# Performance work log

Measured on AMD Instinct MI355X. Metric: run time of the kernel, lower is better.

Reference implementation:

```python
import jax, jax.numpy as jnp
import numpy as np

D_MODEL = 1024
NUM_HEAD = 16
D_HEAD = 64


def setup_inputs() -> dict:
    key = jax.random.key(0)
    ks = jax.random.split(key, 9)
    b, p = 8, 1024
    s = 1.0 / np.sqrt(D_MODEL)
    inp = {
        "x": jax.random.normal(ks[0], (b, p, D_MODEL), jnp.float32),
        "w_q": jax.random.uniform(ks[1], (D_MODEL, D_MODEL), jnp.float32, -s, s),
        "b_q": jax.random.uniform(ks[2], (D_MODEL,), jnp.float32, -s, s),
        "w_k": jax.random.uniform(ks[3], (D_MODEL, D_MODEL), jnp.float32, -s, s),
        "b_k": jax.random.uniform(ks[4], (D_MODEL,), jnp.float32, -s, s),
        "w_v": jax.random.uniform(ks[5], (D_MODEL, D_MODEL), jnp.float32, -s, s),
        "b_v": jax.random.uniform(ks[6], (D_MODEL,), jnp.float32, -s, s),
        "w_o": jax.random.uniform(ks[7], (D_MODEL, D_MODEL), jnp.float32, -s, s),
        "b_o": jax.random.uniform(ks[8], (D_MODEL,), jnp.float32, -s, s),
    }
    return inp


def reference(x, w_q, b_q, w_k, b_k, w_v, b_v, w_o, b_o):
    b, p, _ = x.shape
    # projections (torch Linear: y = x @ W.T + b; here weights stored [in,out])
    q = x @ w_q + b_q
    k = x @ w_k + b_k
    v = x @ w_v + b_v
    # [b, h, p, d]
    q = q.reshape(b, p, NUM_HEAD, D_HEAD).transpose(0, 2, 1, 3)
    k = k.reshape(b, p, NUM_HEAD, D_HEAD).transpose(0, 2, 1, 3)
    v = v.reshape(b, p, NUM_HEAD, D_HEAD).transpose(0, 2, 1, 3)
    scale = 1.0 / np.sqrt(D_HEAD).astype(np.float32)
    scores = jnp.einsum("bhqd,bhkd->bhqk", q, k) * scale
    attn = jax.nn.softmax(scores, axis=-1)
    out = jnp.einsum("bhqk,bhkd->bhqd", attn, v)
    out = out.transpose(0, 2, 1, 3).reshape(b, p, D_MODEL)
    return out @ w_o + b_o
```

## Files before the change

### kernel.cpp

```cpp
#include <hip/hip_runtime.h>
#include <stdint.h>


typedef __attribute__((ext_vector_type(8))) short short8;
typedef __attribute__((ext_vector_type(4))) short s16x4;
typedef __attribute__((ext_vector_type(4))) float f32x4;

__device__ __forceinline__ short f2bf(float f) {
  unsigned u = __builtin_bit_cast(unsigned, f);
  u += 0x7fffu + ((u >> 16) & 1u);
  return (short)(u >> 16);
}

__device__ __forceinline__ unsigned pk2bf(float a, float b) {
  unsigned ua = __builtin_bit_cast(unsigned, a);
  unsigned ub = __builtin_bit_cast(unsigned, b);
  ua += 0x7fffu + ((ua >> 16) & 1u);
  ub += 0x7fffu + ((ub >> 16) & 1u);
  return (ua >> 16) | (ub & 0xffff0000u);
}

__device__ __forceinline__ unsigned cvtpk(float a, float b) {
  unsigned r;
  asm("v_cvt_pk_bf16_f32 %0, %1, %2" : "=v"(r) : "v"(a), "v"(b));
  return r;
}

__device__ __forceinline__ float fexp2(float x) {
  float r;
  asm("v_exp_f32 %0, %1" : "=v"(r) : "v"(x));
  return r;
}

typedef __attribute__((address_space(3))) void lds_void;
typedef __attribute__((address_space(1))) void gbl_void;
#define GLD16(gp, lp) \
  __builtin_amdgcn_global_load_lds((gbl_void*)(gp), (lds_void*)(lp), 16, 0, 0)

#define MFMA(a, b, c) __builtin_amdgcn_mfma_f32_16x16x32_bf16((a), (b), (c), 0, 0, 0)

__global__ __launch_bounds__(256) void k_prep(const float* __restrict__ x,
                                              short* __restrict__ xb,
                                              const float* __restrict__ s0,
                                              const float* __restrict__ s1,
                                              const float* __restrict__ s2,
                                              const float* __restrict__ s3,
                                              short* __restrict__ d0,
                                              short* __restrict__ d1,
                                              short* __restrict__ d2,
                                              short* __restrict__ d3) {
  if (blockIdx.z == 4) {
    int t = threadIdx.y * 32 + threadIdx.x;
    int bid = blockIdx.y * 32 + blockIdx.x;
#pragma unroll
    for (int j = 0; j < 8; ++j) {
      int i = (bid * 2048 + j * 256 + t) * 8;
      const float4* s = (const float4*)(x + i);
      float4 f0 = s[0], f1 = s[1];
      short8 o;
      o[0] = f2bf(f0.x); o[1] = f2bf(f0.y); o[2] = f2bf(f0.z); o[3] = f2bf(f0.w);
      o[4] = f2bf(f1.x); o[5] = f2bf(f1.y); o[6] = f2bf(f1.z); o[7] = f2bf(f1.w);
      *(short8*)(xb + i) = o;
    }
    return;
  }
  __shared__ float tile[64][33];
  const float* srcs[4] = {s0, s1, s2, s3};
  short* dsts[4] = {d0, d1, d2, d3};
  const float* src = srcs[blockIdx.z];
  short* dst = dsts[blockIdx.z];
  int tx = threadIdx.x, ty = threadIdx.y;
  int x0 = blockIdx.x * 32, y0 = blockIdx.y * 64;
#pragma unroll
  for (int i = 0; i < 64; i += 8)
    tile[ty + i][tx] = src[(y0 + ty + i) * 1024 + x0 + tx];
  __syncthreads();
#pragma unroll
  for (int i = 0; i < 32; i += 8) {
    int r = ty + i;
    *(int*)&dst[(x0 + r) * 1024 + y0 + 2 * tx] =
        (int)pk2bf(tile[2 * tx][r], tile[2 * tx + 1][r]);
  }
}

template <int MODE>
__global__ __launch_bounds__(256, 3) void k_gemm(const short* __restrict__ A,
                                                 const short* __restrict__ Bt,
                                                 const float* __restrict__ bias0,
                                                 const float* __restrict__ bias1,
                                                 const float* __restrict__ bias2,
                                                 short* __restrict__ o0,
                                                 short* __restrict__ o1,
                                                 short* __restrict__ o2,
                                                 float* __restrict__ of) {
  __shared__ __align__(16) short a_lds[128 * 64];
  __shared__ __align__(16) short b_lds[128 * 64];
  const int tid = threadIdx.x;
  const int l = blockIdx.x;
  const int m0 = ((((l & 7) << 3) | ((l >> 3) & 7))) << 7;
  const int n0 = (l >> 6) << 7;
  const int w = tid >> 6;
  const int lane = tid & 63;
  const int ll = lane & 15;
  const int qd = lane >> 4;
  const int wm = (w & 1) * 64;
  const int wn = (w >> 1) * 64;

  const int srow = tid >> 3;
  const int schunk = ((tid & 7) ^ (srow & 7)) * 8;
  const short* ag = A + (long)(m0 + srow) * 1024 + schunk;
  const short* bg = Bt + (long)(n0 + srow) * 1024 + schunk;

  f32x4 acc[4][4] = {};

  for (int kt = 0; kt < 1024; kt += 64) {
#pragma unroll
    for (int j = 0; j < 4; ++j) {
      GLD16(ag + j * 32768 + kt, &a_lds[j * 2048 + tid * 8]);
      GLD16(bg + j * 32768 + kt, &b_lds[j * 2048 + tid * 8]);
    }
    __syncthreads();
#pragma unroll
    for (int kh = 0; kh < 2; ++kh) {
      const int xoff = (((kh * 4 + qd) ^ (ll & 7)) * 8);
      short8 af[4], bfr[4];
#pragma unroll
      for (int mt = 0; mt < 4; ++mt)
        af[mt] = *(const short8*)&a_lds[(wm + mt * 16 + ll) * 64 + xoff];
#pragma unroll
      for (int nt = 0; nt < 4; ++nt)
        bfr[nt] = *(const short8*)&b_lds[(wn + nt * 16 + ll) * 64 + xoff];
#pragma unroll
      for (int mt = 0; mt < 4; ++mt)
#pragma unroll
        for (int nt = 0; nt < 4; ++nt)
          acc[mt][nt] = MFMA(af[mt], bfr[nt], acc[mt][nt]);
    }
    __syncthreads();
  }

  if (MODE == 0) {
#pragma unroll
    for (int nt = 0; nt < 4; ++nt) {
      int n = n0 + wn + nt * 16 + ll;
      int which = n >> 10;
      int nl = n & 1023;
      int h = nl >> 6, d = n & 63;
      if (which == 2) {
        float bv = bias2[nl];
        const int b = m0 >> 10;
        const int p0 = (m0 & 1023) + wm;
#pragma unroll
        for (int mt = 0; mt < 4; ++mt) {
          int p = p0 + mt * 16 + qd * 4;
          int2 pk;
          pk.x = (int)pk2bf(acc[mt][nt][0] + bv, acc[mt][nt][1] + bv);
          pk.y = (int)pk2bf(acc[mt][nt][2] + bv, acc[mt][nt][3] + bv);
          *(int2*)&o2[(long)(b * 16 + h) * 65536 + d * 1024 + p] = pk;
        }
      } else {
        float bv = (which == 0) ? bias0[nl] : bias1[nl];
        float sc = (which == 0) ? 0.18033688f : 1.0f;
        short* o = (which == 0) ? o0 : o1;
#pragma unroll
        for (int mt = 0; mt < 4; ++mt) {
#pragma unroll
          for (int r = 0; r < 4; ++r) {
            int m = m0 + wm + mt * 16 + qd * 4 + r;
            int b = m >> 10, p = m & 1023;
            o[(long)(b * 16 + h) * 65536 + p * 64 + d] = f2bf((acc[mt][nt][r] + bv) * sc);
          }
        }
      }
    }
  } else {
#pragma unroll
    for (int nt = 0; nt < 4; ++nt) {
      int n = n0 + wn + nt * 16 + ll;
      float bv = bias0[n];
#pragma unroll
      for (int mt = 0; mt < 4; ++mt) {
#pragma unroll
        for (int r = 0; r < 4; ++r) {
          int m = m0 + wm + mt * 16 + qd * 4 + r;
          of[(long)m * 1024 + n] = acc[mt][nt][r] + bv;
        }
      }
    }
  }
}

__global__ __launch_bounds__(256, 4) void k_attn(const short* __restrict__ Q,
                                                 const short* __restrict__ K,
                                                 const short* __restrict__ VT,
                                                 short* __restrict__ O) {
  __shared__ __align__(16) short k_lds[2][4096];
  __shared__ __align__(16) short vt_lds[2][4096];
  const int tid = threadIdx.x;
  const int w = tid >> 6, lane = tid & 63, ll = lane & 15, qd = lane >> 4;
  const int bid = blockIdx.x;
  const int xcd = bid & 7;
  const int inner = bid >> 3;
  const int bh = xcd * 16 + (inner & 15);
  const int qb = inner >> 4;
  const long hoff = (long)bh * 65536;
  const int qr0 = qb * 128 + w * 32;

  const short* qg = Q + hoff + (long)(qr0 + ll) * 64 + qd * 8;
  short8 qf[2][2];
  qf[0][0] = *(const short8*)qg;
  qf[0][1] = *(const short8*)(qg + 32);
  qf[1][0] = *(const short8*)(qg + 1024);
  qf[1][1] = *(const short8*)(qg + 1024 + 32);

  const int sr = tid >> 3;
  const int swz = (tid & 7) ^ (sr & 7);
  const int pr = (sr & 0x23) | ((sr & 0x0C) << 1) | ((sr & 0x10) >> 2);
  const short* kg = K + hoff + pr * 64 + swz * 8;
  const short* vg = VT + hoff + (long)sr * 1024 + swz * 8;

  const int swzr = ll & 7;
  const int fro0 = ll * 64 + ((qd ^ swzr) * 8);
  const int fro1 = ll * 64 + (((4 + qd) ^ swzr) * 8);

  f32x4 oacc[2][4] = {};
  float l_part[2] = {0.f, 0.f};

  GLD16(kg, &k_lds[0][tid * 8]);
  GLD16(kg + 2048, &k_lds[0][2048 + tid * 8]);
  GLD16(vg, &vt_lds[0][tid * 8]);
  GLD16(vg + 32768, &vt_lds[0][2048 + tid * 8]);
  __syncthreads();

#pragma unroll 2
  for (int c = 0; c < 16; ++c) {
    const int cur = c & 1, nxt = cur ^ 1;
    if (c < 15) {
      GLD16(kg + (c + 1) * 4096, &k_lds[nxt][tid * 8]);
      GLD16(kg + (c + 1) * 4096 + 2048, &k_lds[nxt][2048 + tid * 8]);
      GLD16(vg + (c + 1) * 64, &vt_lds[nxt][tid * 8]);
      GLD16(vg + (c + 1) * 64 + 32768, &vt_lds[nxt][2048 + tid * 8]);
    }

    f32x4 s[2][4];
    __builtin_amdgcn_s_setprio(1);
#pragma unroll
    for (int jt = 0; jt < 4; ++jt) {
      short8 kf0 = *(const short8*)&k_lds[cur][jt * 1024 + fro0];
      short8 kf1 = *(const short8*)&k_lds[cur][jt * 1024 + fro1];
      f32x4 t0 = {};
      t0 = MFMA(kf0, qf[0][0], t0);
      t0 = MFMA(kf1, qf[0][1], t0);
      s[0][jt] = t0;
      f32x4 t1 = {};
      t1 = MFMA(kf0, qf[1][0], t1);
      t1 = MFMA(kf1, qf[1][1], t1);
      s[1][jt] = t1;
    }
    __builtin_amdgcn_s_setprio(0);

    short8 pf[2][2];
#pragma unroll
    for (int g = 0; g < 2; ++g) {
      float rs = 0.f;
#pragma unroll
      for (int jt = 0; jt < 4; ++jt)
#pragma unroll
        for (int r = 0; r < 4; ++r) {
          float e = fexp2(s[g][jt][r]);
          s[g][jt][r] = e;
          rs += e;
        }
      l_part[g] += rs;
#pragma unroll
      for (int u = 0; u < 2; ++u) {
        union { short8 v; unsigned x[4]; } pk;
        pk.x[0] = cvtpk(s[g][2 * u][0], s[g][2 * u][1]);
        pk.x[1] = cvtpk(s[g][2 * u][2], s[g][2 * u][3]);
        pk.x[2] = cvtpk(s[g][2 * u + 1][0], s[g][2 * u + 1][1]);
        pk.x[3] = cvtpk(s[g][2 * u + 1][2], s[g][2 * u + 1][3]);
        pf[g][u] = pk.v;
      }
    }

    __builtin_amdgcn_s_setprio(1);
#pragma unroll
    for (int dt = 0; dt < 4; ++dt) {
      short8 vf0 = *(const short8*)&vt_lds[cur][dt * 1024 + fro0];
      short8 vf1 = *(const short8*)&vt_lds[cur][dt * 1024 + fro1];
      oacc[0][dt] = MFMA(vf0, pf[0][0], oacc[0][dt]);
      oacc[0][dt] = MFMA(vf1, pf[0][1], oacc[0][dt]);
      oacc[1][dt] = MFMA(vf0, pf[1][0], oacc[1][dt]);
      oacc[1][dt] = MFMA(vf1, pf[1][1], oacc[1][dt]);
    }
    __builtin_amdgcn_s_setprio(0);
    __syncthreads();
  }

  const int b = bh >> 4, h = bh & 15;
#pragma unroll
  for (int g = 0; g < 2; ++g) {
    float l = l_part[g];
    l += __shfl_xor(l, 16, 64);
    l += __shfl_xor(l, 32, 64);
    const float inv = 1.0f / l;
    const long row = (long)(b * 1024 + qr0 + g * 16 + ll);
#pragma unroll
    for (int dt = 0; dt < 4; ++dt) {
      int2 ov;
      ov.x = (int)cvtpk(oacc[g][dt][0] * inv, oacc[g][dt][1] * inv);
      ov.y = (int)cvtpk(oacc[g][dt][2] * inv, oacc[g][dt][3] * inv);
      *(int2*)&O[row * 1024 + h * 64 + dt * 16 + qd * 4] = ov;
    }
  }
}

extern "C" void kernel_launch(void* const* d_in, const int* in_sizes, int n_in,
                              void* d_out, int out_size, void* d_ws, size_t ws_size,
                              hipStream_t stream) {
  const float* x   = (const float*)d_in[0];
  const float* w_q = (const float*)d_in[1];
  const float* b_q = (const float*)d_in[2];
  const float* w_k = (const float*)d_in[3];
  const float* b_k = (const float*)d_in[4];
  const float* w_v = (const float*)d_in[5];
  const float* b_v = (const float*)d_in[6];
  const float* w_o = (const float*)d_in[7];
  const float* b_o = (const float*)d_in[8];

  char* ws = (char*)d_ws;
  short* xb    = (short*)(ws);
  short* wqkvT = (short*)(ws + (16ull << 20));
  short* woT   = (short*)(ws + (22ull << 20));
  short* qw    = (short*)(ws + (24ull << 20));
  short* kw    = (short*)(ws + (40ull << 20));
  short* vw    = (short*)(ws + (56ull << 20));

  k_prep<<<dim3(32, 16, 5), dim3(32, 8), 0, stream>>>(
      x, xb, w_q, w_k, w_v, w_o,
      wqkvT, wqkvT + (1 << 20), wqkvT + (2 << 20), woT);

  k_gemm<0><<<1536, 256, 0, stream>>>(xb, wqkvT, b_q, b_k, b_v,
                                      qw, kw, vw, nullptr);

  k_attn<<<dim3(1024), 256, 0, stream>>>(qw, kw, vw, xb);

  k_gemm<1><<<512, 256, 0, stream>>>(xb, woT, b_o, nullptr, nullptr,
                                     nullptr, nullptr, nullptr, (float*)d_out);
}
```

Before: 226.3 us.

## Triple-buffer K/V tiles in attention kernel with prefetch depth two

```diff
diff --git a/kernel.cpp b/kernel.cpp
--- a/kernel.cpp
+++ b/kernel.cpp
@@ -190,12 +190,12 @@
   }
 }
 
-__global__ __launch_bounds__(256, 4) void k_attn(const short* __restrict__ Q,
+__global__ __launch_bounds__(256, 3) void k_attn(const short* __restrict__ Q,
                                                  const short* __restrict__ K,
                                                  const short* __restrict__ VT,
                                                  short* __restrict__ O) {
-  __shared__ __align__(16) short k_lds[2][4096];
-  __shared__ __align__(16) short vt_lds[2][4096];
+  __shared__ __align__(16) short k_lds[3][4096];
+  __shared__ __align__(16) short vt_lds[3][4096];
   const int tid = threadIdx.x;
   const int w = tid >> 6, lane = tid & 63, ll = lane & 15, qd = lane >> 4;
   const int bid = blockIdx.x;
@@ -226,76 +226,84 @@
   f32x4 oacc[2][4] = {};
   float l_part[2] = {0.f, 0.f};
 
-  GLD16(kg, &k_lds[0][tid * 8]);
-  GLD16(kg + 2048, &k_lds[0][2048 + tid * 8]);
-  GLD16(vg, &vt_lds[0][tid * 8]);
-  GLD16(vg + 32768, &vt_lds[0][2048 + tid * 8]);
-  __syncthreads();
-
-#pragma unroll 2
-  for (int c = 0; c < 16; ++c) {
-    const int cur = c & 1, nxt = cur ^ 1;
-    if (c < 15) {
-      GLD16(kg + (c + 1) * 4096, &k_lds[nxt][tid * 8]);
-      GLD16(kg + (c + 1) * 4096 + 2048, &k_lds[nxt][2048 + tid * 8]);
-      GLD16(vg + (c + 1) * 64, &vt_lds[nxt][tid * 8]);
-      GLD16(vg + (c + 1) * 64 + 32768, &vt_lds[nxt][2048 + tid * 8]);
-    }
-
-    f32x4 s[2][4];
-    __builtin_amdgcn_s_setprio(1);
-#pragma unroll
-    for (int jt = 0; jt < 4; ++jt) {
-      short8 kf0 = *(const short8*)&k_lds[cur][jt * 1024 + fro0];
-      short8 kf1 = *(const short8*)&k_lds[cur][jt * 1024 + fro1];
-      f32x4 t0 = {};
-      t0 = MFMA(kf0, qf[0][0], t0);
-      t0 = MFMA(kf1, qf[0][1], t0);
-      s[0][jt] = t0;
-      f32x4 t1 = {};
-      t1 = MFMA(kf0, qf[1][0], t1);
-      t1 = MFMA(kf1, qf[1][1], t1);
-      s[1][jt] = t1;
-    }
-    __builtin_amdgcn_s_setprio(0);
-
-    short8 pf[2][2];
-#pragma unroll
-    for (int g = 0; g < 2; ++g) {
-      float rs = 0.f;
-#pragma unroll
-      for (int jt = 0; jt < 4; ++jt)
-#pragma unroll
-        for (int r = 0; r < 4; ++r) {
-          float e = fexp2(s[g][jt][r]);
-          s[g][jt][r] = e;
-          rs += e;
-        }
-      l_part[g] += rs;
-#pragma unroll
-      for (int u = 0; u < 2; ++u) {
-        union { short8 v; unsigned x[4]; } pk;
-        pk.x[0] = cvtpk(s[g][2 * u][0], s[g][2 * u][1]);
-        pk.x[1] = cvtpk(s[g][2 * u][2], s[g][2 * u][3]);
-        pk.x[2] = cvtpk(s[g][2 * u + 1][0], s[g][2 * u + 1][1]);
-        pk.x[3] = cvtpk(s[g][2 * u + 1][2], s[g][2 * u + 1][3]);
-        pf[g][u] = pk.v;
-      }
-    }
-
-    __builtin_amdgcn_s_setprio(1);
-#pragma unroll
-    for (int dt = 0; dt < 4; ++dt) {
-      short8 vf0 = *(const short8*)&vt_lds[cur][dt * 1024 + fro0];
-      short8 vf1 = *(const short8*)&vt_lds[cur][dt * 1024 + fro1];
-      oacc[0][dt] = MFMA(vf0, pf[0][0], oacc[0][dt]);
-      oacc[0][dt] = MFMA(vf1, pf[0][1], oacc[0][dt]);
-      oacc[1][dt] = MFMA(vf0, pf[1][0], oacc[1][dt]);
-      oacc[1][dt] = MFMA(vf1, pf[1][1], oacc[1][dt]);
-    }
-    __builtin_amdgcn_s_setprio(0);
-    __syncthreads();
-  }
+#define ASTAGE(t, bidx)                                              \
+  {                                                                  \
+    GLD16(kg + (t) * 4096, &k_lds[bidx][tid * 8]);                   \
+    GLD16(kg + (t) * 4096 + 2048, &k_lds[bidx][2048 + tid * 8]);     \
+    GLD16(vg + (t) * 64, &vt_lds[bidx][tid * 8]);                    \
+    GLD16(vg + (t) * 64 + 32768, &vt_lds[bidx][2048 + tid * 8]);     \
+  }
+
+#define ACOMPUTE(cur)                                                        \
+  {                                                                          \
+    f32x4 s[2][4];                                                           \
+    __builtin_amdgcn_s_setprio(1);                                           \
+    _Pragma("unroll")                                                        \
+    for (int jt = 0; jt < 4; ++jt) {                                         \
+      short8 kf0 = *(const short8*)&k_lds[cur][jt * 1024 + fro0];            \
+      short8 kf1 = *(const short8*)&k_lds[cur][jt * 1024 + fro1];            \
+      f32x4 t0 = {};                                                         \
+      t0 = MFMA(kf0, qf[0][0], t0);                                          \
+      t0 = MFMA(kf1, qf[0][1], t0);                                          \
+      s[0][jt] = t0;                                                         \
+      f32x4 t1 = {};                                                         \
+      t1 = MFMA(kf0, qf[1][0], t1);                                          \
+      t1 = MFMA(kf1, qf[1][1], t1);                                          \
+      s[1][jt] = t1;                                                         \
+    }                                                                        \
+    __builtin_amdgcn_s_setprio(0);                                           \
+    short8 pf[2][2];                                                         \
+    _Pragma("unroll")                                                        \
+    for (int g = 0; g < 2; ++g) {                                            \
+      float rs = 0.f;                                                        \
+      _Pragma("unroll")                                                      \
+      for (int jt = 0; jt < 4; ++jt)                                         \
+        _Pragma("unroll")                                                    \
+        for (int r = 0; r < 4; ++r) {                                        \
+          float e = fexp2(s[g][jt][r]);                                      \
+          s[g][jt][r] = e;                                                   \
+          rs += e;                                                           \
+        }                                                                    \
+      l_part[g] += rs;                                                       \
+      _Pragma("unroll")                                                      \
+      for (int u = 0; u < 2; ++u) {                                          \
+        union { short8 v; unsigned x[4]; } pk;                               \
+        pk.x[0] = cvtpk(s[g][2 * u][0], s[g][2 * u][1]);                     \
+        pk.x[1] = cvtpk(s[g][2 * u][2], s[g][2 * u][3]);                     \
+        pk.x[2] = cvtpk(s[g][2 * u + 1][0], s[g][2 * u + 1][1]);             \
+        pk.x[3] = cvtpk(s[g][2 * u + 1][2], s[g][2 * u + 1][3]);             \
+        pf[g][u] = pk.v;                                                     \
+      }                                                                      \
+    }                                                                        \
+    __builtin_amdgcn_s_setprio(1);                                           \
+    _Pragma("unroll")                                                        \
+    for (int dt = 0; dt < 4; ++dt) {                                         \
+      short8 vf0 = *(const short8*)&vt_lds[cur][dt * 1024 + fro0];           \
+      short8 vf1 = *(const short8*)&vt_lds[cur][dt * 1024 + fro1];           \
+      oacc[0][dt] = MFMA(vf0, pf[0][0], oacc[0][dt]);                        \
+      oacc[0][dt] = MFMA(vf1, pf[0][1], oacc[0][dt]);                        \
+      oacc[1][dt] = MFMA(vf0, pf[1][0], oacc[1][dt]);                        \
+      oacc[1][dt] = MFMA(vf1, pf[1][1], oacc[1][dt]);                        \
+    }                                                                        \
+    __builtin_amdgcn_s_setprio(0);                                           \
+  }
+
+  ASTAGE(0, 0);
+  ASTAGE(1, 1);
+
+#pragma unroll 3
+  for (int c = 0; c < 15; ++c) {
+    asm volatile("s_waitcnt vmcnt(4)" ::: "memory");
+    __builtin_amdgcn_s_barrier();
+    if (c < 14) ASTAGE(c + 2, (c + 2) % 3);
+    ACOMPUTE(c % 3);
+  }
+  asm volatile("s_waitcnt vmcnt(0)" ::: "memory");
+  __builtin_amdgcn_s_barrier();
+  ACOMPUTE(0);
+
+#undef ASTAGE
+#undef ACOMPUTE
 
   const int b = bh >> 4, h = bh & 15;
 #pragma unroll
```

After: 237.7 us. +5.1%, slower.
